# Kernel tuning notes

Hardware: AMD Instinct MI355X
Metric: run time of the kernel (lower is better)

## Reference

```python
import jax, jax.numpy as jnp
import numpy as np

DT = 600.0          # integration time step (s)
STEPS = 20          # number of Euler steps
R_EARTH = 6371000.0
DEG2RAD = np.pi / 180.0
KERNEL = jnp.array([[1.0, 2.0, 1.0], [2.0, 4.0, 2.0], [1.0, 2.0, 1.0]], dtype=jnp.float32) / 16.0


def setup_inputs() -> dict:
    key = jax.random.key(0)
    kT, ku, kv, km = jax.random.split(key, 4)
    B, H, W = 8, 360, 720  # 0.5-degree global grid
    T = jax.random.normal(kT, (B, H, W), dtype=jnp.float32)
    ug = jax.random.normal(ku, (B, H, W), dtype=jnp.float32) * 0.5
    vg = jax.random.normal(kv, (B, H, W), dtype=jnp.float32) * 0.5
    lat = (90.0 - 0.25 - jnp.arange(H, dtype=jnp.float32) * 0.5)
    lon = jnp.arange(W, dtype=jnp.float32) * 0.5
    mask = (jax.random.uniform(km, (H, W)) > 0.3).astype(jnp.float32)  # ocean mask
    return {"T": T, "ug": ug, "vg": vg, "lat": lat, "lon": lon, "mask": mask}


def _horizontal_filter(field, mask):
    # field: (B, H, W); 3x3 binomial smoothing, zero ('valid'-style) padding=1, then mask
    k = KERNEL.reshape(1, 1, 3, 3).astype(field.dtype)
    f = jax.lax.conv_general_dilated(field[:, None, :, :], k, window_strides=(1, 1),
                                     padding=((1, 1), (1, 1)))
    return f[:, 0] * mask


def reference(T, ug, vg, lat, lon, mask):
    B, H, W = T.shape
    dlat = lat[1] - lat[0]
    dlon = lon[1] - lon[0]
    dy = R_EARTH * DEG2RAD * jnp.abs(dlat)
    sign_y = jnp.where(dlat > 0, 1.0, -1.0).astype(T.dtype)
    # dx varies with latitude: (H, 1) broadcasts over (B, H, W)
    dx = (R_EARTH * DEG2RAD * dlon) * jnp.cos(lat * DEG2RAD)[:, None]
    maskb = mask[None, :, :]

    def step(Tc, _):
        # boundary-aware meridional derivative
        top = (Tc[:, 1:2, :] - Tc[:, 0:1, :]) / dy
        bot = (Tc[:, -1:, :] - Tc[:, -2:-1, :]) / dy
        mid = (Tc[:, 2:, :] - Tc[:, :-2, :]) / (2.0 * dy)
        dT_dy = jnp.concatenate([top, mid, bot], axis=1) * sign_y
        # periodic zonal derivative
        dT_dx = (jnp.roll(Tc, -1, axis=2) - jnp.roll(Tc, 1, axis=2)) / (2.0 * dx)
        advection = ug * dT_dx + vg * dT_dy
        Tn = Tc - DT * advection * maskb  # Euler update with F = -advection*mask
        Tn = _horizontal_filter(Tn, maskb)
        return Tn, None

    T_final, _ = jax.lax.scan(step, T, None, length=STEPS)
    return T_final
```

## Files before the change

kernel.cpp:

```cpp
#include <hip/hip_runtime.h>

#define H 360
#define W 720
#define NB 8
#define XC 3
#define YC 10
#define TX 240
#define TY 36
#define BPB (XC*YC)
#define WR 52
#define LST 260
#define LSZ (WR*LST)
#define DTS 600.0f
#define REARTH 6371000.0f
#define D2R 0.017453292519943295f

#define NQ1 (WR*64)
#define NHALO 1168
#define NGROUPS 5
#define FLAG_STRIDE 32

static __device__ __forceinline__ float2 ldc8(const float* p) {
    unsigned long long u = __hip_atomic_load((const unsigned long long*)p,
                                             __ATOMIC_RELAXED, __HIP_MEMORY_SCOPE_AGENT);
    return __builtin_bit_cast(float2, u);
}
static __device__ __forceinline__ void stc8(float* p, float2 v) {
    __hip_atomic_store((unsigned long long*)p, __builtin_bit_cast(unsigned long long, v),
                       __ATOMIC_RELAXED, __HIP_MEMORY_SCOPE_AGENT);
}

static __device__ __forceinline__ float dpp_up1(float x) {
    return __builtin_bit_cast(float, __builtin_amdgcn_update_dpp(
        0, __builtin_bit_cast(int, x), 0x138 , 0xF, 0xF, true));
}
static __device__ __forceinline__ float dpp_dn1(float x) {
    return __builtin_bit_cast(float, __builtin_amdgcn_update_dpp(
        0, __builtin_bit_cast(int, x), 0x130 , 0xF, 0xF, true));
}

__global__ __launch_bounds__(512, 2) void ocean_persist(
    const float* __restrict__ Tin, const float* __restrict__ ug,
    const float* __restrict__ vg, const float* __restrict__ lat,
    const float* __restrict__ lon, const float* __restrict__ mask,
    float* __restrict__ out, float* __restrict__ wsf, int* __restrict__ flags)
{
    __shared__ float sT[2 * LSZ];

    const int tid = threadIdx.x;
    const int b  = blockIdx.z;
    const int bx = blockIdx.x * TX;
    const int by = blockIdx.y * TY;
    const int plane = H * W;

    const float dlat = lat[1] - lat[0];
    const float dy   = REARTH * D2R * fabsf(dlat);
    const float sgn  = (dlat > 0.f) ? 1.f : -1.f;
    const float dlon = lon[1] - lon[0];
    const float i2dy = 0.5f / dy, i1dy = 1.f / dy;

    const float* Tb = Tin + b * plane;
    const float* ub = ug  + b * plane;
    const float* vb = vg  + b * plane;
    float* outb = out + b * plane;
    float* wsb  = wsf + b * plane;

    int* bflags = flags + b * BPB * FLAG_STRIDE;
    int* myflag = bflags + (blockIdx.y * XC + blockIdx.x) * FLAG_STRIDE;

    const int cq = tid & 63;
    const int rg = tid >> 6;
    const int c0 = cq << 2;
    const int a  = 1 + 6 * rg;
    const int gj0 = (bx - 8 + c0 + W) % W;
    const bool hlzb = (gj0 == 0);
    const bool hrzb = (gj0 + 3 == W - 1);
    const bool topB = (blockIdx.y == 0), botB = (blockIdx.y == YC - 1);

    int goff1[7], lds1o[7];
    #pragma unroll
    for (int k = 0; k < 7; ++k) {
        const int q = tid + 512 * k;
        if (q < NQ1) {
            const int r = q >> 6, cc0 = (q & 63) << 2;
            int gi = by - 8 + r; gi = min(max(gi, 0), H - 1);
            const int gj = (bx - 8 + cc0 + W) % W;
            goff1[k] = gi * W + gj;
            lds1o[k] = r * LST + cc0;
        } else goff1[k] = -1;
    }

    int hgo[3], hlo[3];
    #pragma unroll
    for (int t = 0; t < 3; ++t) {
        const int q = tid + 512 * t;
        if (q < NHALO) {
            int r, cc0;
            if (q < 1024) { const int ri = q >> 6; r = (ri < 8) ? ri : 36 + ri; cc0 = (q & 63) << 2; }
            else { const int u = q - 1024; r = 8 + (u >> 2); const int qi = u & 3;
                   cc0 = (qi < 2) ? (qi << 2) : (248 + ((qi - 2) << 2)); }
            int gi = by - 8 + r; gi = min(max(gi, 0), H - 1);
            const int gj = (bx - 8 + cc0 + W) % W;
            hgo[t] = gi * W + gj;
            hlo[t] = r * LST + cc0;
        } else hgo[t] = -1;
    }

    float cuA[8][4], cvA[8][4];
    unsigned domm = 0;
    #pragma unroll
    for (int j = 0; j < 8; ++j) {
        #pragma unroll
        for (int t = 0; t < 4; ++t) { cuA[j][t] = 0.f; cvA[j][t] = 0.f; }
        const int gi = by - 8 + a + j;
        if ((unsigned)gi < H) {
            const float dxv  = REARTH * D2R * dlon * cosf(lat[gi] * D2R);
            const float rdx2 = 0.5f / dxv;
            const float ivy  = (gi == 0 || gi == H - 1) ? i1dy : i2dy;
            #pragma unroll
            for (int t = 0; t < 4; ++t) {
                const int off = gi * W + gj0 + t;
                const float mk = mask[off];
                cuA[j][t] = -DTS * mk * ub[off] * rdx2;
                cvA[j][t] = -DTS * mk * vb[off] * sgn * ivy;
            }
            domm |= 1u << j;
        }
    }

    float m16A[6][4];
    int o3A[6];
    unsigned outm = 0, tilem = 0, ringm = 0;
    #pragma unroll
    for (int i = 0; i < 6; ++i) {
        const int n = 2 + 6 * rg + i;
        const int gi = by - 8 + n;
        o3A[i] = 0;
        #pragma unroll
        for (int t = 0; t < 4; ++t)
            m16A[i][t] = ((unsigned)gi < H) ? mask[gi * W + gj0 + t] * (1.f / 16.f) : 0.f;
        if ((unsigned)gi < H) outm |= 1u << i;
        const bool inTile = (n >= 8 && n <= 43 && cq >= 2 && cq <= 61);
        if (inTile) {
            o3A[i] = gi * W + bx + c0 - 8;
            tilem |= 1u << i;
            if (n <= 15 || n >= 36 || cq <= 3 || cq >= 60) ringm |= 1u << i;
        }
    }

    const int* nbrF = myflag;
    if (tid < 8) {
        int dyn, dxn;
        if (tid < 3)      { dyn = -1; dxn = tid - 1; }
        else if (tid == 3){ dyn = 0;  dxn = -1; }
        else if (tid == 4){ dyn = 0;  dxn = 1; }
        else              { dyn = 1;  dxn = tid - 6; }
        const int ny = (int)blockIdx.y + dyn;
        const int nx = ((int)blockIdx.x + dxn + XC) % XC;
        if (ny >= 0 && ny < YC) nbrF = bflags + (ny * XC + nx) * FLAG_STRIDE;
    }

    #pragma unroll
    for (int k = 0; k < 7; ++k)
        if (goff1[k] >= 0) {
            const float4 v = *(const float4*)(Tb + goff1[k]);
            *(float4*)(sT + lds1o[k])       = v;
            *(float4*)(sT + LSZ + lds1o[k]) = v;
        }
    __syncthreads();

    auto substep = [&](int p, bool finalOut, float* ring) {
        const float* cur = sT + p * LSZ;
        float* nxt = sT + (p ^ 1) * LSZ;
        float4 hA[8];
        float4 m1 = *(const float4*)(cur + (a - 1) * LST + c0);
        float4 cc = *(const float4*)(cur + a * LST + c0);
        #pragma unroll
        for (int j = 0; j < 8; ++j) {
            const float4 vD = *(const float4*)(cur + (a + j + 1) * LST + c0);
            const float tl = dpp_up1(cc.w);
            const float tr = dpp_dn1(cc.x);
            const bool dj = (domm >> j) & 1;
            float4 o;
            o.x = (dj ? cc.x : 0.f) + cuA[j][0]*(cc.y - tl)   + cvA[j][0]*(vD.x - m1.x);
            o.y = (dj ? cc.y : 0.f) + cuA[j][1]*(cc.z - cc.x) + cvA[j][1]*(vD.y - m1.y);
            o.z = (dj ? cc.z : 0.f) + cuA[j][2]*(cc.w - cc.y) + cvA[j][2]*(vD.z - m1.z);
            o.w = (dj ? cc.w : 0.f) + cuA[j][3]*(tr   - cc.z) + cvA[j][3]*(vD.w - m1.w);
            float hl = dpp_up1(o.w);
            float hr = dpp_dn1(o.x);
            if (hlzb) hl = 0.f;
            if (hrzb) hr = 0.f;
            hA[j].x = hl  + 2.f * o.x + o.y;
            hA[j].y = o.x + 2.f * o.y + o.z;
            hA[j].z = o.y + 2.f * o.z + o.w;
            hA[j].w = o.z + 2.f * o.w + hr;
            m1 = cc; cc = vD;
        }
        #pragma unroll
        for (int i = 0; i < 6; ++i) {
            const float4 hm = hA[i], hc = hA[i + 1], hp = hA[i + 2];
            float4 o;
            o.x = (hm.x + 2.f * hc.x + hp.x) * m16A[i][0];
            o.y = (hm.y + 2.f * hc.y + hp.y) * m16A[i][1];
            o.z = (hm.z + 2.f * hc.z + hp.z) * m16A[i][2];
            o.w = (hm.w + 2.f * hc.w + hp.w) * m16A[i][3];
            if (!finalOut) {
                if ((outm >> i) & 1)
                    *(float4*)(nxt + (2 + 6 * rg + i) * LST + c0) = o;
                if (topB && rg == 1 && i == 0) *(float4*)(nxt + 7  * LST + c0) = o;
                if (botB && rg == 6 && i == 5) *(float4*)(nxt + 44 * LST + c0) = o;
            } else if ((tilem >> i) & 1) {
                *(float4*)(outb + o3A[i]) = o;
            }
            if (ring && ((ringm >> i) & 1)) {
                float2 lo; lo.x = o.x; lo.y = o.y;
                float2 hi; hi.x = o.z; hi.y = o.w;
                stc8(ring + o3A[i], lo);
                stc8(ring + o3A[i] + 2, hi);
            }
        }
        __syncthreads();
    };

    #pragma unroll 1
    for (int g = 0; g < NGROUPS; ++g) {
        if (g) {
            __syncthreads();
            if (tid == 0)
                __hip_atomic_store(myflag, g, __ATOMIC_RELAXED, __HIP_MEMORY_SCOPE_AGENT);
            if (tid < 64) {
                long long t0 = (long long)clock64();
                for (;;) {
                    const int v = (tid < 8)
                        ? __hip_atomic_load(nbrF, __ATOMIC_RELAXED, __HIP_MEMORY_SCOPE_AGENT)
                        : 0x7fffffff;
                    if (__all(v >= g)) break;
                    __builtin_amdgcn_s_sleep(1);
                    if ((long long)clock64() - t0 > 200000000LL) break;
                }
            }
            __syncthreads();
            const float* prev = ((g - 1) & 1) ? wsb : outb;
            #pragma unroll
            for (int t = 0; t < 3; ++t) {
                if (hgo[t] >= 0) {
                    const float2 lo = ldc8(prev + hgo[t]);
                    const float2 hi = ldc8(prev + hgo[t] + 2);
                    float4 v; v.x = lo.x; v.y = lo.y; v.z = hi.x; v.w = hi.y;
                    *(float4*)(sT + hlo[t]) = v;
                }
            }
            __syncthreads();
        }
        const bool lastG = (g == NGROUPS - 1);
        float* ring = lastG ? nullptr : ((g & 1) ? wsb : outb);
        substep(0, false, nullptr);
        substep(1, false, nullptr);
        substep(0, false, nullptr);
        substep(1, lastG, ring);
    }
}

extern "C" void kernel_launch(void* const* d_in, const int* in_sizes, int n_in,
                              void* d_out, int out_size, void* d_ws, size_t ws_size,
                              hipStream_t stream)
{
    const float* T    = (const float*)d_in[0];
    const float* ug   = (const float*)d_in[1];
    const float* vg   = (const float*)d_in[2];
    const float* lat  = (const float*)d_in[3];
    const float* lon  = (const float*)d_in[4];
    const float* mask = (const float*)d_in[5];
    float* out = (float*)d_out;

    int*   flags = (int*)d_ws;
    float* wsf   = (float*)((char*)d_ws + 65536);

    hipMemsetAsync(d_ws, 0, 65536, stream);

    ocean_persist<<<dim3(XC, YC, NB), dim3(512), 0, stream>>>(
        T, ug, vg, lat, lon, mask, out, wsf, flags);
}
```

Measured before the change: 137.2 us.

## Fuse pairs of time substeps in registers to halve LDS round-trips and barriers

Each pass now computes two consecutive Euler+filter substeps in a streaming register pipeline. The intermediate substep stays in registers, and each thread's row window is widened from 8 to 12 rows, with 10 rows of mask coefficients. This halves the LDS writes/reads and __syncthreads per group of four substeps. In exchange it adds redundant halo-row compute and many more registers (48 more cuA/cvA values), which may lower occupancy or cause spills.

```diff
diff --git a/kernel.cpp b/kernel.cpp
--- a/kernel.cpp
+++ b/kernel.cpp
@@ -20,6 +20,7 @@
 #define NGROUPS 5
 #define FLAG_STRIDE 32
 
+
 static __device__ __forceinline__ float2 ldc8(const float* p) {
     unsigned long long u = __hip_atomic_load((const unsigned long long*)p,
                                              __ATOMIC_RELAXED, __HIP_MEMORY_SCOPE_AGENT);
@@ -71,11 +72,14 @@
     const int cq = tid & 63;
     const int rg = tid >> 6;
     const int c0 = cq << 2;
-    const int a  = 1 + 6 * rg;
+    const int n0 = 6 * rg + 4;
+    const int a1 = 6 * rg + 1;
     const int gj0 = (bx - 8 + c0 + W) % W;
     const bool hlzb = (gj0 == 0);
     const bool hrzb = (gj0 + 3 == W - 1);
     const bool topB = (blockIdx.y == 0), botB = (blockIdx.y == YC - 1);
+    const bool topP = topB && (rg == 0);
+    const bool botP = botB && (rg == 6);
 
     int goff1[7], lds1o[7];
     #pragma unroll
@@ -83,7 +87,7 @@
         const int q = tid + 512 * k;
         if (q < NQ1) {
             const int r = q >> 6, cc0 = (q & 63) << 2;
-            int gi = by - 8 + r; gi = min(max(gi, 0), H - 1);
+            int gi = min(max(by - 8 + r, 0), H - 1);
             const int gj = (bx - 8 + cc0 + W) % W;
             goff1[k] = gi * W + gj;
             lds1o[k] = r * LST + cc0;
@@ -99,20 +103,20 @@
             if (q < 1024) { const int ri = q >> 6; r = (ri < 8) ? ri : 36 + ri; cc0 = (q & 63) << 2; }
             else { const int u = q - 1024; r = 8 + (u >> 2); const int qi = u & 3;
                    cc0 = (qi < 2) ? (qi << 2) : (248 + ((qi - 2) << 2)); }
-            int gi = by - 8 + r; gi = min(max(gi, 0), H - 1);
+            int gi = min(max(by - 8 + r, 0), H - 1);
             const int gj = (bx - 8 + cc0 + W) % W;
             hgo[t] = gi * W + gj;
             hlo[t] = r * LST + cc0;
         } else hgo[t] = -1;
     }
 
-    float cuA[8][4], cvA[8][4];
+    float cuA[12][4], cvA[12][4];
     unsigned domm = 0;
     #pragma unroll
-    for (int j = 0; j < 8; ++j) {
+    for (int k = 0; k < 12; ++k) {
         #pragma unroll
-        for (int t = 0; t < 4; ++t) { cuA[j][t] = 0.f; cvA[j][t] = 0.f; }
-        const int gi = by - 8 + a + j;
+        for (int t = 0; t < 4; ++t) { cuA[k][t] = 0.f; cvA[k][t] = 0.f; }
+        const int gi = by - 8 + a1 + k;
         if ((unsigned)gi < H) {
             const float dxv  = REARTH * D2R * dlon * cosf(lat[gi] * D2R);
             const float rdx2 = 0.5f / dxv;
@@ -121,32 +125,39 @@
             for (int t = 0; t < 4; ++t) {
                 const int off = gi * W + gj0 + t;
                 const float mk = mask[off];
-                cuA[j][t] = -DTS * mk * ub[off] * rdx2;
-                cvA[j][t] = -DTS * mk * vb[off] * sgn * ivy;
-            }
-            domm |= 1u << j;
-        }
-    }
-
-    float m16A[6][4];
-    int o3A[6];
-    unsigned outm = 0, tilem = 0, ringm = 0;
-    #pragma unroll
-    for (int i = 0; i < 6; ++i) {
-        const int n = 2 + 6 * rg + i;
-        const int gi = by - 8 + n;
-        o3A[i] = 0;
+                cuA[k][t] = -DTS * mk * ub[off] * rdx2;
+                cvA[k][t] = -DTS * mk * vb[off] * sgn * ivy;
+            }
+            domm |= 1u << k;
+        }
+    }
+
+    float m16A[10][4];
+    #pragma unroll
+    for (int m = 0; m < 10; ++m) {
+        const int gi = by - 8 + 6 * rg + 2 + m;
         #pragma unroll
         for (int t = 0; t < 4; ++t)
-            m16A[i][t] = ((unsigned)gi < H) ? mask[gi * W + gj0 + t] * (1.f / 16.f) : 0.f;
-        if ((unsigned)gi < H) outm |= 1u << i;
+            m16A[m][t] = ((unsigned)gi < H) ? mask[gi * W + gj0 + t] * (1.f / 16.f) : 0.f;
+    }
+
+    unsigned outmA = 0, outmB = 0, tilem = 0, ringm = 0;
+    #pragma unroll
+    for (int i = 0; i < 6; ++i) {
+        const int n = n0 + i;
+        const int gi = by - 8 + n;
+        if (n <= 47 && (unsigned)gi < H) outmA |= 1u << i;
+        if (n >= 8 && n <= 43)           outmB |= 1u << i;
         const bool inTile = (n >= 8 && n <= 43 && cq >= 2 && cq <= 61);
         if (inTile) {
-            o3A[i] = gi * W + bx + c0 - 8;
             tilem |= 1u << i;
             if (n <= 15 || n >= 36 || cq <= 3 || cq >= 60) ringm |= 1u << i;
         }
     }
+    const int obase = (by - 8 + n0) * W + bx + c0 - 8;
+    const int wbase = n0 * LST + c0;
+    const int rbase = 6 * rg * LST + c0;
+    const int rtop  = 51 * LST + c0;
 
     const int* nbrF = myflag;
     if (tid < 8) {
@@ -169,57 +180,79 @@
         }
     __syncthreads();
 
-    auto substep = [&](int p, bool finalOut, float* ring) {
-        const float* cur = sT + p * LSZ;
-        float* nxt = sT + (p ^ 1) * LSZ;
-        float4 hA[8];
-        float4 m1 = *(const float4*)(cur + (a - 1) * LST + c0);
-        float4 cc = *(const float4*)(cur + a * LST + c0);
+    auto Hrow = [&](int k, const float4& m1, const float4& cc, const float4& vD) -> float4 {
+        const float tl = dpp_up1(cc.w);
+        const float tr = dpp_dn1(cc.x);
+        const bool dj = (domm >> k) & 1;
+        float4 o;
+        o.x = (dj ? cc.x : 0.f) + cuA[k][0]*(cc.y - tl)   + cvA[k][0]*(vD.x - m1.x);
+        o.y = (dj ? cc.y : 0.f) + cuA[k][1]*(cc.z - cc.x) + cvA[k][1]*(vD.y - m1.y);
+        o.z = (dj ? cc.z : 0.f) + cuA[k][2]*(cc.w - cc.y) + cvA[k][2]*(vD.z - m1.z);
+        o.w = (dj ? cc.w : 0.f) + cuA[k][3]*(tr   - cc.z) + cvA[k][3]*(vD.w - m1.w);
+        float hl = dpp_up1(o.w);
+        float hr = dpp_dn1(o.x);
+        if (hlzb) hl = 0.f;
+        if (hrzb) hr = 0.f;
+        float4 r;
+        r.x = hl  + 2.f*o.x + o.y;
+        r.y = o.x + 2.f*o.y + o.z;
+        r.z = o.y + 2.f*o.z + o.w;
+        r.w = o.z + 2.f*o.w + hr;
+        return r;
+    };
+    auto Vrow = [&](int m, const float4& a_, const float4& b_, const float4& c_) -> float4 {
+        float4 r;
+        r.x = (a_.x + 2.f*b_.x + c_.x) * m16A[m][0];
+        r.y = (a_.y + 2.f*b_.y + c_.y) * m16A[m][1];
+        r.z = (a_.z + 2.f*b_.z + c_.z) * m16A[m][2];
+        r.w = (a_.w + 2.f*b_.w + c_.w) * m16A[m][3];
+        return r;
+    };
+
+    auto pair2 = [&](const float* cur, float* nxt, bool isA, bool finalOut, float* ring) {
+        const unsigned wm = isA ? outmA : outmB;
+        float4 z4; z4.x = z4.y = z4.z = z4.w = 0.f;
+        float4 t0 = z4, t1 = z4, h0 = z4, h1 = z4, p0 = z4, p1 = z4, q0 = z4, q1 = z4;
         #pragma unroll
-        for (int j = 0; j < 8; ++j) {
-            const float4 vD = *(const float4*)(cur + (a + j + 1) * LST + c0);
-            const float tl = dpp_up1(cc.w);
-            const float tr = dpp_dn1(cc.x);
-            const bool dj = (domm >> j) & 1;
-            float4 o;
-            o.x = (dj ? cc.x : 0.f) + cuA[j][0]*(cc.y - tl)   + cvA[j][0]*(vD.x - m1.x);
-            o.y = (dj ? cc.y : 0.f) + cuA[j][1]*(cc.z - cc.x) + cvA[j][1]*(vD.y - m1.y);
-            o.z = (dj ? cc.z : 0.f) + cuA[j][2]*(cc.w - cc.y) + cvA[j][2]*(vD.z - m1.z);
-            o.w = (dj ? cc.w : 0.f) + cuA[j][3]*(tr   - cc.z) + cvA[j][3]*(vD.w - m1.w);
-            float hl = dpp_up1(o.w);
-            float hr = dpp_dn1(o.x);
-            if (hlzb) hl = 0.f;
-            if (hrzb) hr = 0.f;
-            hA[j].x = hl  + 2.f * o.x + o.y;
-            hA[j].y = o.x + 2.f * o.y + o.z;
-            hA[j].z = o.y + 2.f * o.z + o.w;
-            hA[j].w = o.z + 2.f * o.w + hr;
-            m1 = cc; cc = vD;
-        }
-        #pragma unroll
-        for (int i = 0; i < 6; ++i) {
-            const float4 hm = hA[i], hc = hA[i + 1], hp = hA[i + 2];
-            float4 o;
-            o.x = (hm.x + 2.f * hc.x + hp.x) * m16A[i][0];
-            o.y = (hm.y + 2.f * hc.y + hp.y) * m16A[i][1];
-            o.z = (hm.z + 2.f * hc.z + hp.z) * m16A[i][2];
-            o.w = (hm.w + 2.f * hc.w + hp.w) * m16A[i][3];
-            if (!finalOut) {
-                if ((outm >> i) & 1)
-                    *(float4*)(nxt + (2 + 6 * rg + i) * LST + c0) = o;
-                if (topB && rg == 1 && i == 0) *(float4*)(nxt + 7  * LST + c0) = o;
-                if (botB && rg == 6 && i == 5) *(float4*)(nxt + 44 * LST + c0) = o;
-            } else if ((tilem >> i) & 1) {
-                *(float4*)(outb + o3A[i]) = o;
-            }
-            if (ring && ((ringm >> i) & 1)) {
-                float2 lo; lo.x = o.x; lo.y = o.y;
-                float2 hi; hi.x = o.z; hi.y = o.w;
-                stc8(ring + o3A[i], lo);
-                stc8(ring + o3A[i] + 2, hi);
-            }
-        }
-        __syncthreads();
+        for (int s = 0; s < 14; ++s) {
+            const int off = min(rbase + s * LST, rtop);
+            const float4 tn = *(const float4*)(cur + off);
+            float4 hn = z4, pn = z4, qn = z4;
+            if (s >= 2) hn = Hrow(s - 2, t0, t1, tn);
+            if (s >= 4) pn = Vrow(s - 4, h0, h1, hn);
+            if (s >= 6) {
+                const int k2 = s - 6;
+                float4 m1q = p0, vDq = pn;
+                if (topP && k2 == 5) m1q = p1;
+                if (botP && k2 == 4) vDq = p1;
+                qn = Hrow(k2 + 2, m1q, p1, vDq);
+            }
+            if (s >= 8) {
+                const int i = s - 8;
+                const float4 o = Vrow(i + 2, q0, q1, qn);
+                if (!finalOut) {
+                    if ((wm >> i) & 1)
+                        *(float4*)(nxt + wbase + i * LST) = o;
+                    if (isA) {
+                        if (topP && i == 4) *(float4*)(nxt + 7  * LST + c0) = o;
+                        if (botB && rg == 6 && i == 3)
+                                            *(float4*)(nxt + 44 * LST + c0) = o;
+                    }
+                } else if ((tilem >> i) & 1) {
+                    *(float4*)(outb + obase + i * W) = o;
+                }
+                if (ring && ((ringm >> i) & 1)) {
+                    float2 lo; lo.x = o.x; lo.y = o.y;
+                    float2 hi; hi.x = o.z; hi.y = o.w;
+                    stc8(ring + obase + i * W, lo);
+                    stc8(ring + obase + i * W + 2, hi);
+                }
+            }
+            t0 = t1; t1 = tn;
+            if (s >= 2) { h0 = h1; h1 = hn; }
+            if (s >= 4) { p0 = p1; p1 = pn; }
+            if (s >= 6) { q0 = q1; q1 = qn; }
+        }
     };
 
     #pragma unroll 1
@@ -229,14 +262,14 @@
             if (tid == 0)
                 __hip_atomic_store(myflag, g, __ATOMIC_RELAXED, __HIP_MEMORY_SCOPE_AGENT);
             if (tid < 64) {
-                long long t0 = (long long)clock64();
+                long long t0c = (long long)clock64();
                 for (;;) {
                     const int v = (tid < 8)
                         ? __hip_atomic_load(nbrF, __ATOMIC_RELAXED, __HIP_MEMORY_SCOPE_AGENT)
                         : 0x7fffffff;
                     if (__all(v >= g)) break;
                     __builtin_amdgcn_s_sleep(1);
-                    if ((long long)clock64() - t0 > 200000000LL) break;
+                    if ((long long)clock64() - t0c > 200000000LL) break;
                 }
             }
             __syncthreads();
@@ -253,11 +286,11 @@
             __syncthreads();
         }
         const bool lastG = (g == NGROUPS - 1);
-        float* ring = lastG ? nullptr : ((g & 1) ? wsb : outb);
-        substep(0, false, nullptr);
-        substep(1, false, nullptr);
-        substep(0, false, nullptr);
-        substep(1, lastG, ring);
+        float* ringp = lastG ? nullptr : ((g & 1) ? wsb : outb);
+        pair2(sT, sT + LSZ, true, false, nullptr);
+        __syncthreads();
+        pair2(sT + LSZ, sT, false, lastG, ringp);
+        __syncthreads();
     }
 }
 
```

Result: slower. 248.0 us (+80.7%).
